# Kernel tuning notes

Measured on AMD Instinct MI355X. Metric: run time of the kernel, lower is better.

The kernel has to match this reference:

```python
import jax, jax.numpy as jnp
import numpy as np

IN_F, OUT_F, K = 1024, 1024, 12
EPS = 1e-6


def setup_inputs() -> dict:
    key = jax.random.key(0)
    k1, k2, k3, k4 = jax.random.split(key, 4)
    x = jax.random.normal(k1, (4, 4096, IN_F), dtype=jnp.float32)
    # grid: linspace(-2,2,K) per feature + small noise so sort is nontrivial
    base = jnp.linspace(-2.0, 2.0, K, dtype=jnp.float32)
    grid = base[None, :] + 0.1 * jax.random.normal(k2, (IN_F, K), dtype=jnp.float32)
    coeffs = 0.1 * jax.random.normal(k3, (IN_F, K), dtype=jnp.float32)
    tangents = jnp.zeros((IN_F, K), dtype=jnp.float32)
    knot_alive = jnp.full((IN_F, K), 3.0, dtype=jnp.float32)
    kw1, kw2 = jax.random.split(k4)
    proj_w = jax.random.normal(kw1, (OUT_F, IN_F), dtype=jnp.float32) / np.sqrt(IN_F)
    proj_b = jnp.zeros((OUT_F,), dtype=jnp.float32)
    res_w = jax.random.normal(kw2, (OUT_F, IN_F), dtype=jnp.float32) / np.sqrt(IN_F)
    return {"x": x, "grid": grid, "coeffs": coeffs, "tangents": tangents,
            "knot_alive": knot_alive, "proj_w": proj_w, "proj_b": proj_b, "res_w": res_w}


def _eval_hermite_spline(x, grid, coeffs, tangents, knot_alive):
    # sort knots per input feature (grid: [F,K])
    sort_idx = jnp.argsort(grid, axis=1)
    sorted_grid = jnp.take_along_axis(grid, sort_idx, axis=1)
    sorted_coeffs = jnp.take_along_axis(coeffs, sort_idx, axis=1)
    sorted_tangents = jnp.take_along_axis(tangents, sort_idx, axis=1)
    sorted_alive = jnp.take_along_axis(knot_alive, sort_idx, axis=1)
    alive = jax.nn.sigmoid(sorted_alive)
    mc = sorted_coeffs * alive          # masked heights [F,K]
    mt = sorted_tangents * alive        # masked tangents [F,K]

    orig_shape = x.shape
    xf = x.reshape(-1, orig_shape[-1])  # [M,F]
    gmin = sorted_grid[:, 0]            # [F]
    gmax = sorted_grid[:, -1]
    xc = jnp.clip(xf, gmin[None, :], gmax[None, :])
    grange = jnp.maximum(gmax - gmin, EPS)
    xn = (xc - gmin[None, :]) / grange[None, :] * (K - 1)  # [M,F]
    idx_l = jnp.clip(xn.astype(jnp.int32), 0, K - 2)
    t = xn - idx_l.astype(xf.dtype)

    feat = jnp.arange(xf.shape[1])[None, :]  # [1,F] broadcast against [M,F] idx
    p0 = mc[feat, idx_l]
    p1 = mc[feat, idx_l + 1]
    m0 = mt[feat, idx_l]
    m1 = mt[feat, idx_l + 1]
    x_left = sorted_grid[feat, idx_l]
    x_right = sorted_grid[feat, idx_l + 1]
    dx = jnp.maximum(x_right - x_left, EPS)

    t2 = t * t
    t3 = t2 * t
    h00 = 2 * t3 - 3 * t2 + 1
    h10 = t3 - 2 * t2 + t
    h01 = -2 * t3 + 3 * t2
    h11 = t3 - t2
    out = h00 * p0 + h10 * m0 * dx + h01 * p1 + h11 * m1 * dx
    return out.reshape(orig_shape)


def reference(x, grid, coeffs, tangents, knot_alive, proj_w, proj_b, res_w):
    spline_out = _eval_hermite_spline(x, grid, coeffs, tangents, knot_alive)
    # proj(spline_out) + residual(x); torch Linear: y = x @ W.T + b
    return (jnp.einsum('...i,oi->...o', spline_out, proj_w) + proj_b
            + jnp.einsum('...i,oi->...o', x, res_w))
```

## Files before the change

kernel.cpp:

```cpp
#include <hip/hip_runtime.h>
#include <hip/hip_bf16.h>


#define IN_F   1024
#define OUT_F  1024
#define KNOTS  12
#define M_ROWS 16384
#define GK     2048

#define BM   256
#define BN   256
#define BKT  64
#define NTK  (GK / BKT)

typedef __attribute__((ext_vector_type(8))) __bf16 bf16x8;
typedef __attribute__((ext_vector_type(4))) float  f32x4;

__device__ __forceinline__ unsigned short f2bf(float v) {
    unsigned int u = __float_as_uint(v);
    u = (u + 0x7fffu + ((u >> 16) & 1u)) >> 16;
    return (unsigned short)u;
}

__device__ __forceinline__ void gload16(const void* g, void* l) {
    __builtin_amdgcn_global_load_lds(
        (const __attribute__((address_space(1))) void*)g,
        (__attribute__((address_space(3))) void*)l, 16, 0, 0);
}

__global__ __launch_bounds__(256) void prep_kernel(
    const float* __restrict__ grid, const float* __restrict__ coeffs,
    const float* __restrict__ tangents, const float* __restrict__ alive,
    float* __restrict__ gmin, float* __restrict__ scale, float4* __restrict__ H)
{
    int f = blockIdx.x * blockDim.x + threadIdx.x;
    if (f >= IN_F) return;
    float g[KNOTS], c[KNOTS], t[KNOTS], a[KNOTS];
    for (int i = 0; i < KNOTS; ++i) {
        g[i] = grid[f*KNOTS+i];  c[i] = coeffs[f*KNOTS+i];
        t[i] = tangents[f*KNOTS+i]; a[i] = alive[f*KNOTS+i];
    }
    for (int i = 1; i < KNOTS; ++i) {
        float gk=g[i], ck=c[i], tk=t[i], ak=a[i];
        int j = i-1;
        while (j >= 0 && g[j] > gk) { g[j+1]=g[j]; c[j+1]=c[j]; t[j+1]=t[j]; a[j+1]=a[j]; --j; }
        g[j+1]=gk; c[j+1]=ck; t[j+1]=tk; a[j+1]=ak;
    }
    float mcl[KNOTS], mtl[KNOTS];
    for (int i = 0; i < KNOTS; ++i) {
        float s = 1.f / (1.f + expf(-a[i]));
        mcl[i] = c[i]*s;  mtl[i] = t[i]*s;
    }
    gmin[f] = g[0];
    float grange = fmaxf(g[KNOTS-1] - g[0], 1e-6f);
    scale[f] = (float)(KNOTS-1) / grange;
    for (int k = 0; k < KNOTS-1; ++k) {
        float dx = fmaxf(g[k+1]-g[k], 1e-6f);
        H[(size_t)f*KNOTS + k] = make_float4(mcl[k], mcl[k+1], mtl[k]*dx, mtl[k+1]*dx);
    }
    H[(size_t)f*KNOTS + KNOTS-1] = make_float4(0.f, 0.f, 0.f, 0.f);
}

#define SROWS 64
#define HPAD  13
__global__ __launch_bounds__(256) void spline_kernel(const float* __restrict__ x,
    const float* __restrict__ gmin, const float* __restrict__ scale,
    const float4* __restrict__ H, unsigned short* __restrict__ A)
{
    __shared__ float4 sH[256 * HPAD];
    __shared__ float  sGm[256], sSc[256];
    const int tid  = threadIdx.x;
    const int fblk = blockIdx.y * 256;
    #pragma unroll
    for (int k = 0; k < KNOTS; ++k) sH[tid*HPAD + k] = H[(size_t)(fblk+tid)*KNOTS + k];
    sGm[tid] = gmin[fblk+tid];
    sSc[tid] = scale[fblk+tid];
    __syncthreads();

    const int wave = tid >> 6, lane = tid & 63;
    const int f0 = lane * 4;
    const float4 gm4 = *reinterpret_cast<const float4*>(&sGm[f0]);
    const float4 sc4 = *reinterpret_cast<const float4*>(&sSc[f0]);
    const float gms[4] = {gm4.x, gm4.y, gm4.z, gm4.w};
    const float scs[4] = {sc4.x, sc4.y, sc4.z, sc4.w};
    const int r0 = blockIdx.x * SROWS;

    #pragma unroll 2
    for (int r = wave; r < SROWS; r += 4) {
        const int row = r0 + r;
        const float4 xv = *reinterpret_cast<const float4*>(x + (size_t)row*IN_F + fblk + f0);
        const float xs[4] = {xv.x, xv.y, xv.z, xv.w};
        ushort4 so, xo;
        unsigned short* sp = (unsigned short*)&so;
        unsigned short* xp = (unsigned short*)&xo;
        #pragma unroll
        for (int j = 0; j < 4; ++j) {
            const float xi = xs[j];
            float xn = (xi - gms[j]) * scs[j];
            xn = fminf(fmaxf(xn, 0.f), (float)(KNOTS-1));
            int idx = (int)xn;  idx = idx > (KNOTS-2) ? (KNOTS-2) : idx;
            const float tt = xn - (float)idx;
            const float4 h = sH[(f0+j)*HPAD + idx];
            const float t2 = tt*tt, t3 = t2*tt;
            const float h00 =  2.f*t3 - 3.f*t2 + 1.f;
            const float h01 = -2.f*t3 + 3.f*t2;
            const float h10 =  t3 - 2.f*t2 + tt;
            const float h11 =  t3 - t2;
            sp[j] = f2bf(h00*h.x + h01*h.y + h10*h.z + h11*h.w);
            xp[j] = f2bf(xi);
        }
        const size_t base = (size_t)row * GK + fblk + f0;
        *reinterpret_cast<ushort4*>(A + base)        = so;
        *reinterpret_cast<ushort4*>(A + base + IN_F) = xo;
    }
}

__global__ __launch_bounds__(256) void bcast_kernel(
    const float* __restrict__ P, const float* __restrict__ R,
    unsigned short* __restrict__ Bc)
{
    int g = blockIdx.x*256 + threadIdx.x;
    int n  = g >> 9;
    int k4 = (g & 511) * 4;
    const float* src = (k4 < IN_F) ? (P + (size_t)n*IN_F + k4)
                                   : (R + (size_t)n*IN_F + (k4 - IN_F));
    float4 v = *reinterpret_cast<const float4*>(src);
    ushort4 o;
    o.x = f2bf(v.x); o.y = f2bf(v.y); o.z = f2bf(v.z); o.w = f2bf(v.w);
    *reinterpret_cast<ushort4*>(Bc + (size_t)n*GK + k4) = o;
}

__global__ __launch_bounds__(512, 2) void gemm_kernel(
    const unsigned short* __restrict__ A, const unsigned short* __restrict__ B,
    const float* __restrict__ bias, float* __restrict__ C)
{
    __shared__ unsigned short sA[2][2][128*64];
    __shared__ unsigned short sB[2][2][128*64];

    const int tid  = threadIdx.x;
    const int wg   = blockIdx.x;
    const int swzb = (wg & 7) * 32 + (wg >> 3);
    const int by   = swzb >> 2;
    const int bx   = swzb & 3;

    const int lane = tid & 63;
    const int wave = tid >> 6;
    const int wr   = wave >> 2;
    const int wc   = wave & 3;
    const int lr   = lane & 15;
    const int lsl  = lane >> 4;

    const size_t aRow0 = (size_t)by * BM;
    const size_t bRow0 = (size_t)bx * BN;

    auto stage = [&](const unsigned short* __restrict__ G, size_t gRow0,
                     unsigned short* lds, int ts) {
        const int k0 = ts * BKT;
        #pragma unroll
        for (int i = 0; i < 2; ++i) {
            const int L16 = i*512 + tid;
            const int lrow = L16 >> 3;
            const int ss = (L16 & 7) ^ (lrow & 7);
            gload16(G + (gRow0 + lrow)*GK + k0 + ss*8, lds + (size_t)L16*8);
        }
    };
    auto rd = [&](const unsigned short* s, int lrow, int ks) -> bf16x8 {
        const int sp = (ks*4 + lsl) ^ (lrow & 7);
        return *reinterpret_cast<const bf16x8*>(s + lrow*64 + sp*8);
    };

    f32x4 acc[8][4] = {};
    bf16x8 a[4][2], bb[2][2][2];

    stage(A, aRow0,       &sA[0][0][0], 0);
    stage(B, bRow0,       &sB[0][0][0], 0);
    stage(A, aRow0 + 128, &sA[0][1][0], 0);
    stage(B, bRow0 + 128, &sB[0][1][0], 0);
    stage(A, aRow0,       &sA[1][0][0], 1);
    stage(B, bRow0,       &sB[1][0][0], 1);
    asm volatile("s_waitcnt vmcnt(8)" ::: "memory");
    __builtin_amdgcn_s_barrier();

    for (int t = 0; t < NTK; ++t) {
        const int b = t & 1;
        unsigned short* sA0 = &sA[b][0][0];
        unsigned short* sA1 = &sA[b][1][0];
        unsigned short* sB0 = &sB[b][0][0];
        unsigned short* sB1 = &sB[b][1][0];

        #pragma unroll
        for (int m = 0; m < 4; ++m)
            #pragma unroll
            for (int ks = 0; ks < 2; ++ks)
                a[m][ks] = rd(sA0, wr*64 + m*16 + lr, ks);
        #pragma unroll
        for (int n = 0; n < 2; ++n)
            #pragma unroll
            for (int ks = 0; ks < 2; ++ks)
                bb[0][n][ks] = rd(sB0, wc*32 + n*16 + lr, ks);
        if (t+1 < NTK) stage(A, aRow0 + 128, &sA[b^1][1][0], t+1);
        if (t == NTK-1) asm volatile("s_waitcnt vmcnt(0)" ::: "memory");
        else            asm volatile("s_waitcnt vmcnt(6)" ::: "memory");
        __builtin_amdgcn_s_barrier();
        __builtin_amdgcn_s_setprio(1);
        #pragma unroll
        for (int m = 0; m < 4; ++m)
          #pragma unroll
          for (int n = 0; n < 2; ++n)
            #pragma unroll
            for (int ks = 0; ks < 2; ++ks)
                acc[m][n] = __builtin_amdgcn_mfma_f32_16x16x32_bf16(a[m][ks], bb[0][n][ks], acc[m][n], 0, 0, 0);
        __builtin_amdgcn_s_setprio(0);
        __builtin_amdgcn_s_barrier();

        #pragma unroll
        for (int n = 0; n < 2; ++n)
            #pragma unroll
            for (int ks = 0; ks < 2; ++ks)
                bb[1][n][ks] = rd(sB1, wc*32 + n*16 + lr, ks);
        if (t+1 < NTK) stage(B, bRow0 + 128, &sB[b^1][1][0], t+1);
        asm volatile("s_waitcnt vmcnt(10)" ::: "memory");
        __builtin_amdgcn_s_barrier();
        __builtin_amdgcn_s_setprio(1);
        #pragma unroll
        for (int m = 0; m < 4; ++m)
          #pragma unroll
          for (int n = 0; n < 2; ++n)
            #pragma unroll
            for (int ks = 0; ks < 2; ++ks)
                acc[m][2+n] = __builtin_amdgcn_mfma_f32_16x16x32_bf16(a[m][ks], bb[1][n][ks], acc[m][2+n], 0, 0, 0);
        __builtin_amdgcn_s_setprio(0);
        __builtin_amdgcn_s_barrier();

        #pragma unroll
        for (int m = 0; m < 4; ++m)
            #pragma unroll
            for (int ks = 0; ks < 2; ++ks)
                a[m][ks] = rd(sA1, wr*64 + m*16 + lr, ks);
        if (t+2 < NTK) stage(A, aRow0, &sA[b][0][0], t+2);
        __builtin_amdgcn_s_barrier();
        __builtin_amdgcn_s_setprio(1);
        #pragma unroll
        for (int m = 0; m < 4; ++m)
          #pragma unroll
          for (int n = 0; n < 2; ++n)
            #pragma unroll
            for (int ks = 0; ks < 2; ++ks)
                acc[4+m][n] = __builtin_amdgcn_mfma_f32_16x16x32_bf16(a[m][ks], bb[0][n][ks], acc[4+m][n], 0, 0, 0);
        __builtin_amdgcn_s_setprio(0);
        __builtin_amdgcn_s_barrier();

        if (t+2 < NTK) stage(B, bRow0, &sB[b][0][0], t+2);
        if (t == NTK-2) asm volatile("s_waitcnt vmcnt(4)" ::: "memory");
        else            asm volatile("s_waitcnt vmcnt(8)" ::: "memory");
        __builtin_amdgcn_s_barrier();
        __builtin_amdgcn_s_setprio(1);
        #pragma unroll
        for (int m = 0; m < 4; ++m)
          #pragma unroll
          for (int n = 0; n < 2; ++n)
            #pragma unroll
            for (int ks = 0; ks < 2; ++ks)
                acc[4+m][2+n] = __builtin_amdgcn_mfma_f32_16x16x32_bf16(a[m][ks], bb[1][n][ks], acc[4+m][2+n], 0, 0, 0);
        __builtin_amdgcn_s_setprio(0);
        __builtin_amdgcn_s_barrier();
    }

    #pragma unroll
    for (int nh = 0; nh < 2; ++nh)
      #pragma unroll
      for (int n = 0; n < 2; ++n) {
        const int col = bx*BN + nh*128 + wc*32 + n*16 + lr;
        const float bv = bias[col];
        #pragma unroll
        for (int mh = 0; mh < 2; ++mh)
          #pragma unroll
          for (int m = 0; m < 4; ++m) {
            const int grow = by*BM + mh*128 + wr*64 + m*16 + lsl*4;
            #pragma unroll
            for (int r = 0; r < 4; ++r)
                C[(size_t)(grow + r)*OUT_F + col] = acc[mh*4+m][nh*2+n][r] + bv;
          }
      }
}

__global__ __launch_bounds__(256) void fallback_kernel(
    const float* __restrict__ x, const float* __restrict__ P,
    const float* __restrict__ R, const float* __restrict__ pb,
    const float* __restrict__ gmin, const float* __restrict__ scale,
    const float4* __restrict__ H, float* __restrict__ out)
{
    __shared__ float s_s[IN_F];
    __shared__ float s_x[IN_F];
    int row = blockIdx.x;
    const float* xr = x + (size_t)row*IN_F;
    for (int f = threadIdx.x; f < IN_F; f += 256) {
        float xi = xr[f];
        float xn = (xi - gmin[f]) * scale[f];
        xn = fminf(fmaxf(xn, 0.f), (float)(KNOTS-1));
        int idx = (int)xn;  idx = idx > (KNOTS-2) ? (KNOTS-2) : idx;
        float tt = xn - (float)idx;
        float4 h = H[(size_t)f*KNOTS + idx];
        float t2 = tt*tt, t3 = t2*tt;
        s_s[f] = (2.f*t3-3.f*t2+1.f)*h.x + (-2.f*t3+3.f*t2)*h.y
               + (t3-2.f*t2+tt)*h.z + (t3-t2)*h.w;
        s_x[f] = xi;
    }
    __syncthreads();
    for (int j = 0; j < 4; ++j) {
        int o = threadIdx.x + j*256;
        const float* Pr = P + (size_t)o*IN_F;
        const float* Rr = R + (size_t)o*IN_F;
        float acc = pb[o];
        for (int f = 0; f < IN_F; ++f)
            acc = fmaf(s_s[f], Pr[f], fmaf(s_x[f], Rr[f], acc));
        out[(size_t)row*OUT_F + o] = acc;
    }
}

extern "C" void kernel_launch(void* const* d_in, const int* in_sizes, int n_in,
                              void* d_out, int out_size, void* d_ws, size_t ws_size,
                              hipStream_t stream) {
    const float* x         = (const float*)d_in[0];
    const float* grid      = (const float*)d_in[1];
    const float* coeffs    = (const float*)d_in[2];
    const float* tangents  = (const float*)d_in[3];
    const float* knotalive = (const float*)d_in[4];
    const float* proj_w    = (const float*)d_in[5];
    const float* proj_b    = (const float*)d_in[6];
    const float* res_w     = (const float*)d_in[7];
    float* out = (float*)d_out;

    const size_t needB  = (size_t)OUT_F * GK * 2;
    const size_t needA  = (size_t)M_ROWS * GK * 2;
    const size_t needT  = ((size_t)IN_F*2 + (size_t)IN_F*KNOTS*4) * 4;

    char* ws = (char*)d_ws;
    if (ws_size >= needB + needA + needT) {
        unsigned short* Bcat = (unsigned short*)ws;
        unsigned short* Abuf = (unsigned short*)(ws + needB);
        float*  gmin = (float*)(ws + needB + needA);
        float*  scl  = gmin + IN_F;
        float4* H    = (float4*)(scl + IN_F);

        prep_kernel<<<(IN_F+255)/256, 256, 0, stream>>>(grid, coeffs, tangents, knotalive,
                                                        gmin, scl, H);
        bcast_kernel<<<(OUT_F*GK/4)/256, 256, 0, stream>>>(proj_w, res_w, Bcat);
        spline_kernel<<<dim3(M_ROWS/SROWS, IN_F/256), 256, 0, stream>>>(x, gmin, scl, H, Abuf);
        gemm_kernel<<<(M_ROWS/BM)*(OUT_F/BN), 512, 0, stream>>>(Abuf, Bcat, proj_b, out);
    } else {
        float*  gmin = (float*)ws;
        float*  scl  = gmin + IN_F;
        float4* H    = (float4*)(scl + IN_F);
        prep_kernel<<<(IN_F+255)/256, 256, 0, stream>>>(grid, coeffs, tangents, knotalive,
                                                        gmin, scl, H);
        fallback_kernel<<<M_ROWS, 256, 0, stream>>>(x, proj_w, res_w, proj_b,
                                                    gmin, scl, H, out);
    }
}
```

Before: 107.0 us.

## Switch GEMM to 32x32x16 MFMA with simpler double-buffered K pipeline

Replaces the 16x16x32 MFMA tiling with 32x32x16 bf16 MFMAs, so each wave computes a 128x64 sub-tile as 4x2 32x32 accumulators. The interleaved half-tile staging schedule, with its fine-grained vmcnt waits and many barriers, is replaced by a plain double buffer that prefetches the whole next K-tile and waits on vmcnt(0) once per iteration. This cuts LDS reads per MFMA and removes barrier overhead. In exchange, global-load latency is only hidden behind one tile of compute, and the epilogue writes to C with a strided 32x32 output pattern.

```diff
diff --git a/kernel.cpp b/kernel.cpp
--- a/kernel.cpp
+++ b/kernel.cpp
@@ -13,8 +13,9 @@
 #define BKT  64
 #define NTK  (GK / BKT)
 
-typedef __attribute__((ext_vector_type(8))) __bf16 bf16x8;
-typedef __attribute__((ext_vector_type(4))) float  f32x4;
+typedef __attribute__((ext_vector_type(8)))  __bf16 bf16x8;
+typedef __attribute__((ext_vector_type(4)))  float  f32x4;
+typedef __attribute__((ext_vector_type(16))) float  f32x16;
 
 __device__ __forceinline__ unsigned short f2bf(float v) {
     unsigned int u = __float_as_uint(v);
@@ -134,8 +135,8 @@
     const unsigned short* __restrict__ A, const unsigned short* __restrict__ B,
     const float* __restrict__ bias, float* __restrict__ C)
 {
-    __shared__ unsigned short sA[2][2][128*64];
-    __shared__ unsigned short sB[2][2][128*64];
+    __shared__ unsigned short sA[2][BM*BKT];
+    __shared__ unsigned short sB[2][BN*BKT];
 
     const int tid  = threadIdx.x;
     const int wg   = blockIdx.x;
@@ -147,8 +148,8 @@
     const int wave = tid >> 6;
     const int wr   = wave >> 2;
     const int wc   = wave & 3;
-    const int lr   = lane & 15;
-    const int lsl  = lane >> 4;
+    const int l31  = lane & 31;
+    const int hi   = lane >> 5;
 
     const size_t aRow0 = (size_t)by * BM;
     const size_t bRow0 = (size_t)bx * BN;
@@ -157,131 +158,98 @@
                      unsigned short* lds, int ts) {
         const int k0 = ts * BKT;
         #pragma unroll
-        for (int i = 0; i < 2; ++i) {
-            const int L16 = i*512 + tid;
+        for (int i = 0; i < 4; ++i) {
+            const int L16  = i*512 + tid;
             const int lrow = L16 >> 3;
-            const int ss = (L16 & 7) ^ (lrow & 7);
+            const int ss   = (L16 & 7) ^ (lrow & 7);
             gload16(G + (gRow0 + lrow)*GK + k0 + ss*8, lds + (size_t)L16*8);
         }
     };
-    auto rd = [&](const unsigned short* s, int lrow, int ks) -> bf16x8 {
-        const int sp = (ks*4 + lsl) ^ (lrow & 7);
-        return *reinterpret_cast<const bf16x8*>(s + lrow*64 + sp*8);
+    auto rd = [&](const unsigned short* s, int row, int ks16) -> bf16x8 {
+        const int sp = (ks16*2 + hi) ^ (row & 7);
+        return *reinterpret_cast<const bf16x8*>(s + row*BKT + sp*8);
     };
 
-    f32x4 acc[8][4] = {};
-    bf16x8 a[4][2], bb[2][2][2];
-
-    stage(A, aRow0,       &sA[0][0][0], 0);
-    stage(B, bRow0,       &sB[0][0][0], 0);
-    stage(A, aRow0 + 128, &sA[0][1][0], 0);
-    stage(B, bRow0 + 128, &sB[0][1][0], 0);
-    stage(A, aRow0,       &sA[1][0][0], 1);
-    stage(B, bRow0,       &sB[1][0][0], 1);
-    asm volatile("s_waitcnt vmcnt(8)" ::: "memory");
-    __builtin_amdgcn_s_barrier();
+    f32x16 acc[4][2] = {};
+
+    stage(A, aRow0, &sA[0][0], 0);
+    stage(B, bRow0, &sB[0][0], 0);
 
     for (int t = 0; t < NTK; ++t) {
         const int b = t & 1;
-        unsigned short* sA0 = &sA[b][0][0];
-        unsigned short* sA1 = &sA[b][1][0];
-        unsigned short* sB0 = &sB[b][0][0];
-        unsigned short* sB1 = &sB[b][1][0];
-
-        #pragma unroll
-        for (int m = 0; m < 4; ++m)
-            #pragma unroll
-            for (int ks = 0; ks < 2; ++ks)
-                a[m][ks] = rd(sA0, wr*64 + m*16 + lr, ks);
-        #pragma unroll
-        for (int n = 0; n < 2; ++n)
-            #pragma unroll
-            for (int ks = 0; ks < 2; ++ks)
-                bb[0][n][ks] = rd(sB0, wc*32 + n*16 + lr, ks);
-        if (t+1 < NTK) stage(A, aRow0 + 128, &sA[b^1][1][0], t+1);
-        if (t == NTK-1) asm volatile("s_waitcnt vmcnt(0)" ::: "memory");
-        else            asm volatile("s_waitcnt vmcnt(6)" ::: "memory");
+        const unsigned short* cA = &sA[b][0];
+        const unsigned short* cB = &sB[b][0];
+
+        asm volatile("s_waitcnt vmcnt(0)" ::: "memory");
         __builtin_amdgcn_s_barrier();
-        __builtin_amdgcn_s_setprio(1);
-        #pragma unroll
-        for (int m = 0; m < 4; ++m)
-          #pragma unroll
-          for (int n = 0; n < 2; ++n)
-            #pragma unroll
-            for (int ks = 0; ks < 2; ++ks)
-                acc[m][n] = __builtin_amdgcn_mfma_f32_16x16x32_bf16(a[m][ks], bb[0][n][ks], acc[m][n], 0, 0, 0);
-        __builtin_amdgcn_s_setprio(0);
-        __builtin_amdgcn_s_barrier();
-
-        #pragma unroll
-        for (int n = 0; n < 2; ++n)
-            #pragma unroll
-            for (int ks = 0; ks < 2; ++ks)
-                bb[1][n][ks] = rd(sB1, wc*32 + n*16 + lr, ks);
-        if (t+1 < NTK) stage(B, bRow0 + 128, &sB[b^1][1][0], t+1);
-        asm volatile("s_waitcnt vmcnt(10)" ::: "memory");
-        __builtin_amdgcn_s_barrier();
-        __builtin_amdgcn_s_setprio(1);
-        #pragma unroll
-        for (int m = 0; m < 4; ++m)
-          #pragma unroll
-          for (int n = 0; n < 2; ++n)
-            #pragma unroll
-            for (int ks = 0; ks < 2; ++ks)
-                acc[m][2+n] = __builtin_amdgcn_mfma_f32_16x16x32_bf16(a[m][ks], bb[1][n][ks], acc[m][2+n], 0, 0, 0);
-        __builtin_amdgcn_s_setprio(0);
-        __builtin_amdgcn_s_barrier();
-
-        #pragma unroll
-        for (int m = 0; m < 4; ++m)
-            #pragma unroll
-            for (int ks = 0; ks < 2; ++ks)
-                a[m][ks] = rd(sA1, wr*64 + m*16 + lr, ks);
-        if (t+2 < NTK) stage(A, aRow0, &sA[b][0][0], t+2);
-        __builtin_amdgcn_s_barrier();
-        __builtin_amdgcn_s_setprio(1);
-        #pragma unroll
-        for (int m = 0; m < 4; ++m)
-          #pragma unroll
-          for (int n = 0; n < 2; ++n)
-            #pragma unroll
-            for (int ks = 0; ks < 2; ++ks)
-                acc[4+m][n] = __builtin_amdgcn_mfma_f32_16x16x32_bf16(a[m][ks], bb[0][n][ks], acc[4+m][n], 0, 0, 0);
-        __builtin_amdgcn_s_setprio(0);
-        __builtin_amdgcn_s_barrier();
-
-        if (t+2 < NTK) stage(B, bRow0, &sB[b][0][0], t+2);
-        if (t == NTK-2) asm volatile("s_waitcnt vmcnt(4)" ::: "memory");
-        else            asm volatile("s_waitcnt vmcnt(8)" ::: "memory");
-        __builtin_amdgcn_s_barrier();
-        __builtin_amdgcn_s_setprio(1);
-        #pragma unroll
-        for (int m = 0; m < 4; ++m)
-          #pragma unroll
-          for (int n = 0; n < 2; ++n)
-            #pragma unroll
-            for (int ks = 0; ks < 2; ++ks)
-                acc[4+m][2+n] = __builtin_amdgcn_mfma_f32_16x16x32_bf16(a[m][ks], bb[1][n][ks], acc[4+m][2+n], 0, 0, 0);
-        __builtin_amdgcn_s_setprio(0);
-        __builtin_amdgcn_s_barrier();
+
+        {
+            bf16x8 av[4][2], bv[2][2];
+            #pragma unroll
+            for (int m = 0; m < 4; ++m)
+                #pragma unroll
+                for (int s = 0; s < 2; ++s)
+                    av[m][s] = rd(cA, wr*128 + m*32 + l31, s);
+            #pragma unroll
+            for (int n = 0; n < 2; ++n)
+                #pragma unroll
+                for (int s = 0; s < 2; ++s)
+                    bv[n][s] = rd(cB, wc*64 + n*32 + l31, s);
+            if (t + 1 < NTK) {
+                stage(A, aRow0, &sA[b^1][0], t+1);
+                stage(B, bRow0, &sB[b^1][0], t+1);
+            }
+            __builtin_amdgcn_s_setprio(1);
+            #pragma unroll
+            for (int m = 0; m < 4; ++m)
+              #pragma unroll
+              for (int n = 0; n < 2; ++n)
+                #pragma unroll
+                for (int s = 0; s < 2; ++s)
+                    acc[m][n] = __builtin_amdgcn_mfma_f32_32x32x16_bf16(
+                        av[m][s], bv[n][s], acc[m][n], 0, 0, 0);
+            __builtin_amdgcn_s_setprio(0);
+        }
+
+        {
+            bf16x8 av[4][2], bv[2][2];
+            #pragma unroll
+            for (int m = 0; m < 4; ++m)
+                #pragma unroll
+                for (int s = 0; s < 2; ++s)
+                    av[m][s] = rd(cA, wr*128 + m*32 + l31, 2+s);
+            #pragma unroll
+            for (int n = 0; n < 2; ++n)
+                #pragma unroll
+                for (int s = 0; s < 2; ++s)
+                    bv[n][s] = rd(cB, wc*64 + n*32 + l31, 2+s);
+            __builtin_amdgcn_s_setprio(1);
+            #pragma unroll
+            for (int m = 0; m < 4; ++m)
+              #pragma unroll
+              for (int n = 0; n < 2; ++n)
+                #pragma unroll
+                for (int s = 0; s < 2; ++s)
+                    acc[m][n] = __builtin_amdgcn_mfma_f32_32x32x16_bf16(
+                        av[m][s], bv[n][s], acc[m][n], 0, 0, 0);
+            __builtin_amdgcn_s_setprio(0);
+        }
     }
 
     #pragma unroll
-    for (int nh = 0; nh < 2; ++nh)
-      #pragma unroll
-      for (int n = 0; n < 2; ++n) {
-        const int col = bx*BN + nh*128 + wc*32 + n*16 + lr;
+    for (int n = 0; n < 2; ++n) {
+        const int col = bx*BN + wc*64 + n*32 + l31;
         const float bv = bias[col];
         #pragma unroll
-        for (int mh = 0; mh < 2; ++mh)
-          #pragma unroll
-          for (int m = 0; m < 4; ++m) {
-            const int grow = by*BM + mh*128 + wr*64 + m*16 + lsl*4;
-            #pragma unroll
-            for (int r = 0; r < 4; ++r)
-                C[(size_t)(grow + r)*OUT_F + col] = acc[mh*4+m][nh*2+n][r] + bv;
-          }
-      }
+        for (int m = 0; m < 4; ++m) {
+            const int rowbase = by*BM + wr*128 + m*32 + 4*hi;
+            #pragma unroll
+            for (int q = 0; q < 4; ++q)
+                #pragma unroll
+                for (int r = 0; r < 4; ++r)
+                    C[(size_t)(rowbase + 8*q + r)*OUT_F + col] = acc[m][n][q*4+r] + bv;
+        }
+    }
 }
 
 __global__ __launch_bounds__(256) void fallback_kernel(
```

Result: slower. 116.3 us (+8.7%).

## Fuse spline evaluation into GEMM A-tile staging and interleave K layout

Applied to the files above, without the earlier changes.

Removes the separate spline kernel and its bf16 A buffer. The GEMM now loads fp32 x rows directly, evaluates the Hermite spline in registers, and writes both the spline and x halves into swizzled LDS tiles. The weight concat is reordered so each 64-wide K tile holds 32 projection and 32 residual columns. This cuts the large intermediate write and re-read but puts the spline ALU work and fp32 loads inside the GEMM's pipeline, which can stall the MFMA schedule. It also changes the vmcnt/lgkmcnt wait accounting.

```diff
diff --git a/kernel.cpp b/kernel.cpp
--- a/kernel.cpp
+++ b/kernel.cpp
@@ -14,6 +14,7 @@
 #define NTK  (GK / BKT)
 
 typedef __attribute__((ext_vector_type(8))) __bf16 bf16x8;
+typedef __attribute__((ext_vector_type(8))) unsigned short u16x8;
 typedef __attribute__((ext_vector_type(4))) float  f32x4;
 
 __device__ __forceinline__ unsigned short f2bf(float v) {
@@ -31,7 +32,8 @@
 __global__ __launch_bounds__(256) void prep_kernel(
     const float* __restrict__ grid, const float* __restrict__ coeffs,
     const float* __restrict__ tangents, const float* __restrict__ alive,
-    float* __restrict__ gmin, float* __restrict__ scale, float4* __restrict__ H)
+    float* __restrict__ gmin, float* __restrict__ scale,
+    float4* __restrict__ H, float2* __restrict__ gs)
 {
     int f = blockIdx.x * blockDim.x + threadIdx.x;
     if (f >= IN_F) return;
@@ -54,65 +56,12 @@
     gmin[f] = g[0];
     float grange = fmaxf(g[KNOTS-1] - g[0], 1e-6f);
     scale[f] = (float)(KNOTS-1) / grange;
+    gs[f] = make_float2(g[0], (float)(KNOTS-1) / grange);
     for (int k = 0; k < KNOTS-1; ++k) {
         float dx = fmaxf(g[k+1]-g[k], 1e-6f);
         H[(size_t)f*KNOTS + k] = make_float4(mcl[k], mcl[k+1], mtl[k]*dx, mtl[k+1]*dx);
     }
     H[(size_t)f*KNOTS + KNOTS-1] = make_float4(0.f, 0.f, 0.f, 0.f);
-}
-
-#define SROWS 64
-#define HPAD  13
-__global__ __launch_bounds__(256) void spline_kernel(const float* __restrict__ x,
-    const float* __restrict__ gmin, const float* __restrict__ scale,
-    const float4* __restrict__ H, unsigned short* __restrict__ A)
-{
-    __shared__ float4 sH[256 * HPAD];
-    __shared__ float  sGm[256], sSc[256];
-    const int tid  = threadIdx.x;
-    const int fblk = blockIdx.y * 256;
-    #pragma unroll
-    for (int k = 0; k < KNOTS; ++k) sH[tid*HPAD + k] = H[(size_t)(fblk+tid)*KNOTS + k];
-    sGm[tid] = gmin[fblk+tid];
-    sSc[tid] = scale[fblk+tid];
-    __syncthreads();
-
-    const int wave = tid >> 6, lane = tid & 63;
-    const int f0 = lane * 4;
-    const float4 gm4 = *reinterpret_cast<const float4*>(&sGm[f0]);
-    const float4 sc4 = *reinterpret_cast<const float4*>(&sSc[f0]);
-    const float gms[4] = {gm4.x, gm4.y, gm4.z, gm4.w};
-    const float scs[4] = {sc4.x, sc4.y, sc4.z, sc4.w};
-    const int r0 = blockIdx.x * SROWS;
-
-    #pragma unroll 2
-    for (int r = wave; r < SROWS; r += 4) {
-        const int row = r0 + r;
-        const float4 xv = *reinterpret_cast<const float4*>(x + (size_t)row*IN_F + fblk + f0);
-        const float xs[4] = {xv.x, xv.y, xv.z, xv.w};
-        ushort4 so, xo;
-        unsigned short* sp = (unsigned short*)&so;
-        unsigned short* xp = (unsigned short*)&xo;
-        #pragma unroll
-        for (int j = 0; j < 4; ++j) {
-            const float xi = xs[j];
-            float xn = (xi - gms[j]) * scs[j];
-            xn = fminf(fmaxf(xn, 0.f), (float)(KNOTS-1));
-            int idx = (int)xn;  idx = idx > (KNOTS-2) ? (KNOTS-2) : idx;
-            const float tt = xn - (float)idx;
-            const float4 h = sH[(f0+j)*HPAD + idx];
-            const float t2 = tt*tt, t3 = t2*tt;
-            const float h00 =  2.f*t3 - 3.f*t2 + 1.f;
-            const float h01 = -2.f*t3 + 3.f*t2;
-            const float h10 =  t3 - 2.f*t2 + tt;
-            const float h11 =  t3 - t2;
-            sp[j] = f2bf(h00*h.x + h01*h.y + h10*h.z + h11*h.w);
-            xp[j] = f2bf(xi);
-        }
-        const size_t base = (size_t)row * GK + fblk + f0;
-        *reinterpret_cast<ushort4*>(A + base)        = so;
-        *reinterpret_cast<ushort4*>(A + base + IN_F) = xo;
-    }
 }
 
 __global__ __launch_bounds__(256) void bcast_kernel(
@@ -121,21 +70,25 @@
 {
     int g = blockIdx.x*256 + threadIdx.x;
     int n  = g >> 9;
-    int k4 = (g & 511) * 4;
-    const float* src = (k4 < IN_F) ? (P + (size_t)n*IN_F + k4)
-                                   : (R + (size_t)n*IN_F + (k4 - IN_F));
+    int c4 = (g & 511) * 4;
+    int t  = c4 >> 6, j = c4 & 63;
+    const float* src = (j < 32) ? (P + (size_t)n*IN_F + t*32 + j)
+                                : (R + (size_t)n*IN_F + t*32 + (j - 32));
     float4 v = *reinterpret_cast<const float4*>(src);
     ushort4 o;
     o.x = f2bf(v.x); o.y = f2bf(v.y); o.z = f2bf(v.z); o.w = f2bf(v.w);
-    *reinterpret_cast<ushort4*>(Bc + (size_t)n*GK + k4) = o;
+    *reinterpret_cast<ushort4*>(Bc + (size_t)n*GK + c4) = o;
 }
 
 __global__ __launch_bounds__(512, 2) void gemm_kernel(
-    const unsigned short* __restrict__ A, const unsigned short* __restrict__ B,
+    const float* __restrict__ X, const unsigned short* __restrict__ B,
+    const float4* __restrict__ H, const float2* __restrict__ GS,
     const float* __restrict__ bias, float* __restrict__ C)
 {
     __shared__ unsigned short sA[2][2][128*64];
     __shared__ unsigned short sB[2][2][128*64];
+    __shared__ float4 sHt[2][32*12];
+    __shared__ float2 sGt[2][32];
 
     const int tid  = threadIdx.x;
     const int wg   = blockIdx.x;
@@ -153,16 +106,53 @@
     const size_t aRow0 = (size_t)by * BM;
     const size_t bRow0 = (size_t)bx * BN;
 
-    auto stage = [&](const unsigned short* __restrict__ G, size_t gRow0,
-                     unsigned short* lds, int ts) {
-        const int k0 = ts * BKT;
+    auto stageB = [&](int t, int buf, int half) {
+        const int k0 = t * BKT;
         #pragma unroll
         for (int i = 0; i < 2; ++i) {
             const int L16 = i*512 + tid;
             const int lrow = L16 >> 3;
             const int ss = (L16 & 7) ^ (lrow & 7);
-            gload16(G + (gRow0 + lrow)*GK + k0 + ss*8, lds + (size_t)L16*8);
-        }
+            gload16(B + (bRow0 + half*128 + lrow)*GK + k0 + ss*8,
+                    &sB[buf][half][(size_t)L16*8]);
+        }
+    };
+    auto stageH = [&](int kt, int hb) {
+        if (tid < 384)       gload16(H + (size_t)kt*384 + tid, &sHt[hb][tid]);
+        else if (tid < 400)  gload16(GS + (size_t)kt*32 + (tid-384)*2, &sGt[hb][(tid-384)*2]);
+    };
+    auto loadx = [&](int kt, int half, float4& v0, float4& v1) {
+        const float* p = X + (aRow0 + half*128 + (tid>>2))*IN_F + kt*32 + (tid&3)*8;
+        v0 = *reinterpret_cast<const float4*>(p);
+        v1 = *reinterpret_cast<const float4*>(p + 4);
+    };
+    auto evalwrite = [&](int hb, unsigned short* dst, float4 v0, float4 v1) {
+        const int row = tid >> 2, q = tid & 3;
+        float gm[8], sc[8];
+        #pragma unroll
+        for (int e = 0; e < 8; e += 2) {
+            float4 g2 = *reinterpret_cast<const float4*>(&sGt[hb][q*8 + e]);
+            gm[e] = g2.x; sc[e] = g2.y; gm[e+1] = g2.z; sc[e+1] = g2.w;
+        }
+        const float xs[8] = {v0.x,v0.y,v0.z,v0.w,v1.x,v1.y,v1.z,v1.w};
+        u16x8 so, xo;
+        #pragma unroll
+        for (int e = 0; e < 8; ++e) {
+            const float xi = xs[e];
+            float xn = (xi - gm[e]) * sc[e];
+            xn = fminf(fmaxf(xn, 0.f), (float)(KNOTS-1));
+            int idx = (int)xn;  idx = idx > (KNOTS-2) ? (KNOTS-2) : idx;
+            const float tt = xn - (float)idx;
+            const float4 h = sHt[hb][(q*8+e)*12 + idx];
+            const float t2 = tt*tt, t3 = t2*tt;
+            so[e] = (unsigned short)f2bf((2.f*t3-3.f*t2+1.f)*h.x + (-2.f*t3+3.f*t2)*h.y
+                                       + (t3-2.f*t2+tt)*h.z + (t3-t2)*h.w);
+            xo[e] = (unsigned short)f2bf(xi);
+        }
+        const int ps = q ^ (row & 7);
+        const int pr = (4 + q) ^ (row & 7);
+        *reinterpret_cast<u16x8*>(dst + row*64 + ps*8) = so;
+        *reinterpret_cast<u16x8*>(dst + row*64 + pr*8) = xo;
     };
     auto rd = [&](const unsigned short* s, int lrow, int ks) -> bf16x8 {
         const int sp = (ks*4 + lsl) ^ (lrow & 7);
@@ -172,21 +162,28 @@
     f32x4 acc[8][4] = {};
     bf16x8 a[4][2], bb[2][2][2];
 
-    stage(A, aRow0,       &sA[0][0][0], 0);
-    stage(B, bRow0,       &sB[0][0][0], 0);
-    stage(A, aRow0 + 128, &sA[0][1][0], 0);
-    stage(B, bRow0 + 128, &sB[0][1][0], 0);
-    stage(A, aRow0,       &sA[1][0][0], 1);
-    stage(B, bRow0,       &sB[1][0][0], 1);
-    asm volatile("s_waitcnt vmcnt(8)" ::: "memory");
+    stageH(0, 0); stageH(1, 1);
+    stageB(0, 0, 0); stageB(0, 0, 1); stageB(1, 1, 0);
+    {
+        float4 v0, v1;
+        loadx(0, 0, v0, v1);
+        asm volatile("s_waitcnt vmcnt(0)" ::: "memory");
+        evalwrite(0, &sA[0][0][0], v0, v1);
+        loadx(0, 1, v0, v1);
+        evalwrite(0, &sA[0][1][0], v0, v1);
+        loadx(1, 0, v0, v1);
+        evalwrite(1, &sA[1][0][0], v0, v1);
+    }
+    asm volatile("s_waitcnt lgkmcnt(0)" ::: "memory");
     __builtin_amdgcn_s_barrier();
 
     for (int t = 0; t < NTK; ++t) {
         const int b = t & 1;
-        unsigned short* sA0 = &sA[b][0][0];
-        unsigned short* sA1 = &sA[b][1][0];
-        unsigned short* sB0 = &sB[b][0][0];
-        unsigned short* sB1 = &sB[b][1][0];
+        const unsigned short* sA0 = &sA[b][0][0];
+        const unsigned short* sA1 = &sA[b][1][0];
+        const unsigned short* sB0 = &sB[b][0][0];
+        const unsigned short* sB1 = &sB[b][1][0];
+        float4 xA1_0, xA1_1, xA0_0, xA0_1;
 
         #pragma unroll
         for (int m = 0; m < 4; ++m)
@@ -198,9 +195,10 @@
             #pragma unroll
             for (int ks = 0; ks < 2; ++ks)
                 bb[0][n][ks] = rd(sB0, wc*32 + n*16 + lr, ks);
-        if (t+1 < NTK) stage(A, aRow0 + 128, &sA[b^1][1][0], t+1);
+        if (t+2 < NTK) stageH(t+2, t & 1);
+        if (t+1 < NTK) loadx(t+1, 1, xA1_0, xA1_1);
         if (t == NTK-1) asm volatile("s_waitcnt vmcnt(0)" ::: "memory");
-        else            asm volatile("s_waitcnt vmcnt(6)" ::: "memory");
+        else            asm volatile("s_waitcnt vmcnt(4)" ::: "memory");
         __builtin_amdgcn_s_barrier();
         __builtin_amdgcn_s_setprio(1);
         #pragma unroll
@@ -218,8 +216,11 @@
             #pragma unroll
             for (int ks = 0; ks < 2; ++ks)
                 bb[1][n][ks] = rd(sB1, wc*32 + n*16 + lr, ks);
-        if (t+1 < NTK) stage(B, bRow0 + 128, &sB[b^1][1][0], t+1);
-        asm volatile("s_waitcnt vmcnt(10)" ::: "memory");
+        if (t+1 < NTK) {
+            evalwrite((t+1) & 1, &sA[b^1][1][0], xA1_0, xA1_1);
+            stageB(t+1, b^1, 1);
+        }
+        asm volatile("s_waitcnt lgkmcnt(0)" ::: "memory");
         __builtin_amdgcn_s_barrier();
         __builtin_amdgcn_s_setprio(1);
         #pragma unroll
@@ -237,7 +238,8 @@
             #pragma unroll
             for (int ks = 0; ks < 2; ++ks)
                 a[m][ks] = rd(sA1, wr*64 + m*16 + lr, ks);
-        if (t+2 < NTK) stage(A, aRow0, &sA[b][0][0], t+2);
+        if (t+2 < NTK) loadx(t+2, 0, xA0_0, xA0_1);
+        asm volatile("s_waitcnt vmcnt(2)" ::: "memory");
         __builtin_amdgcn_s_barrier();
         __builtin_amdgcn_s_setprio(1);
         #pragma unroll
@@ -250,9 +252,13 @@
         __builtin_amdgcn_s_setprio(0);
         __builtin_amdgcn_s_barrier();
 
-        if (t+2 < NTK) stage(B, bRow0, &sB[b][0][0], t+2);
-        if (t == NTK-2) asm volatile("s_waitcnt vmcnt(4)" ::: "memory");
-        else            asm volatile("s_waitcnt vmcnt(8)" ::: "memory");
+        if (t+2 < NTK) {
+            evalwrite(t & 1, &sA[b][0][0], xA0_0, xA0_1);
+            stageB(t+2, b, 0);
+        }
+        asm volatile("s_waitcnt lgkmcnt(0)" ::: "memory");
+        if (t >= NTK-2) asm volatile("s_waitcnt vmcnt(0)" ::: "memory");
+        else            asm volatile("s_waitcnt vmcnt(4)" ::: "memory");
         __builtin_amdgcn_s_barrier();
         __builtin_amdgcn_s_setprio(1);
         #pragma unroll
@@ -332,28 +338,23 @@
     float* out = (float*)d_out;
 
     const size_t needB  = (size_t)OUT_F * GK * 2;
-    const size_t needA  = (size_t)M_ROWS * GK * 2;
-    const size_t needT  = ((size_t)IN_F*2 + (size_t)IN_F*KNOTS*4) * 4;
+    const size_t needT  = ((size_t)IN_F*2 + (size_t)IN_F*KNOTS*4 + (size_t)IN_F*2) * 4;
 
     char* ws = (char*)d_ws;
-    if (ws_size >= needB + needA + needT) {
-        unsigned short* Bcat = (unsigned short*)ws;
-        unsigned short* Abuf = (unsigned short*)(ws + needB);
-        float*  gmin = (float*)(ws + needB + needA);
-        float*  scl  = gmin + IN_F;
-        float4* H    = (float4*)(scl + IN_F);
-
+    unsigned short* Bcat = (unsigned short*)ws;
+    float*  gmin = (float*)(ws + needB);
+    float*  scl  = gmin + IN_F;
+    float4* H    = (float4*)(scl + IN_F);
+    float2* gs   = (float2*)(H + (size_t)IN_F*KNOTS);
+
+    if (ws_size >= needB + needT) {
         prep_kernel<<<(IN_F+255)/256, 256, 0, stream>>>(grid, coeffs, tangents, knotalive,
-                                                        gmin, scl, H);
+                                                        gmin, scl, H, gs);
         bcast_kernel<<<(OUT_F*GK/4)/256, 256, 0, stream>>>(proj_w, res_w, Bcat);
-        spline_kernel<<<dim3(M_ROWS/SROWS, IN_F/256), 256, 0, stream>>>(x, gmin, scl, H, Abuf);
-        gemm_kernel<<<(M_ROWS/BM)*(OUT_F/BN), 512, 0, stream>>>(Abuf, Bcat, proj_b, out);
+        gemm_kernel<<<(M_ROWS/BM)*(OUT_F/BN), 512, 0, stream>>>(x, Bcat, H, gs, proj_b, out);
     } else {
-        float*  gmin = (float*)ws;
-        float*  scl  = gmin + IN_F;
-        float4* H    = (float4*)(scl + IN_F);
         prep_kernel<<<(IN_F+255)/256, 256, 0, stream>>>(grid, coeffs, tangents, knotalive,
-                                                        gmin, scl, H);
+                                                        gmin, scl, H, gs);
         fallback_kernel<<<M_ROWS, 256, 0, stream>>>(x, proj_w, res_w, proj_b,
                                                     gmin, scl, H, out);
     }
```

After: 173.1 us. +61.8%, slower.
